# Kernel tuning notes

Measured on AMD Instinct MI355X. Metric: run time of the kernel, lower is better.

Reference implementation:

```python
import jax, jax.numpy as jnp
import numpy as np

N_COARSE = 64
N_FINE = 64
EPS = 1e-5

BS, N_RAYS = 1, 131072


def setup_inputs() -> dict:
    key = jax.random.key(0)
    k0, k1, k2, k3, k4, k5 = jax.random.split(key, 6)
    origins = jax.random.normal(k0, (BS, N_RAYS, 3), dtype=jnp.float32)
    dirs = jax.random.normal(k1, (BS, N_RAYS, 3), dtype=jnp.float32)
    dirs = dirs / jnp.linalg.norm(dirs, axis=-1, keepdims=True)
    near = 2.0 + 0.5 * jax.random.uniform(k2, (BS, N_RAYS, 1), dtype=jnp.float32)
    far = 6.0 + 0.5 * jax.random.uniform(k3, (BS, N_RAYS, 1), dtype=jnp.float32)
    rays = jnp.concatenate([origins, dirs, near, far], axis=-1)  # (bs, n_rays, 8)
    sigmas_coarse = jax.random.normal(k4, (BS, N_RAYS, N_COARSE), dtype=jnp.float32)
    rgbs_coarse = jax.random.uniform(k5, (BS, N_RAYS, N_COARSE, 3), dtype=jnp.float32)
    k6, k7 = jax.random.split(jax.random.fold_in(key, 1), 2)
    sigmas_fine = jax.random.normal(k6, (BS, N_RAYS, N_COARSE + N_FINE), dtype=jnp.float32)
    rgbs_fine = jax.random.uniform(k7, (BS, N_RAYS, N_COARSE + N_FINE, 3), dtype=jnp.float32)
    return {
        "rays": rays,
        "sigmas_coarse": sigmas_coarse,
        "rgbs_coarse": rgbs_coarse,
        "sigmas_fine": sigmas_fine,
        "rgbs_fine": rgbs_fine,
    }


def composite(rays, z_samp, sigmas, rgbs):
    """Alpha compositing along the sample axis (white background, far=inf)."""
    deltas = z_samp[..., 1:] - z_samp[..., :-1]
    delta_inf = jnp.full_like(deltas[..., :1], 1e10)
    deltas = jnp.concatenate([deltas, delta_inf], axis=-1)  # (bs, n_rays, K)
    alphas = 1.0 - jnp.exp(-deltas * jax.nn.relu(sigmas))
    shifted = jnp.concatenate(
        [jnp.ones_like(alphas[..., :1]), 1.0 - alphas + 1e-10], axis=-1)
    T = jnp.cumprod(shifted, axis=-1)  # transmittance
    weights = alphas * T[..., :-1]
    weights_sum = jnp.sum(weights, axis=-1, keepdims=True)
    rgb_final = jnp.sum(weights[..., None] * rgbs, axis=-2)
    depth_final = jnp.sum(weights * z_samp, axis=-1, keepdims=True)
    far = rays[..., 7:8]
    depth_final = depth_final + (1.0 - weights_sum) * far  # white_bkgd
    rgb_final = rgb_final + 1.0 - weights_sum
    return weights, rgb_final, depth_final, weights_sum


def sample_fine(bins, weights):
    """Deterministic inverse-CDF importance sampling (det=True, perturb=0)."""
    bs, n_rays = bins.shape[:2]
    w = jax.lax.stop_gradient(weights) + EPS  # (bs, n_rays, Kc-2)
    pdf = w / jnp.sum(w, axis=-1, keepdims=True)
    cdf = jnp.cumsum(pdf, axis=-1)
    cdf = jnp.concatenate([jnp.zeros_like(cdf[..., :1]), cdf], axis=-1)  # (.., Kc-1)
    u = jnp.broadcast_to(jnp.linspace(0.0, 1.0, N_FINE, dtype=cdf.dtype),
                         (bs, n_rays, N_FINE))
    n_bins = cdf.shape[-1]
    inds = jax.vmap(lambda c, uu: jnp.searchsorted(c, uu, side='right'))(
        cdf.reshape(-1, n_bins), u.reshape(-1, N_FINE)).reshape(bs, n_rays, N_FINE)
    below = jnp.maximum(inds - 1, 0)
    above = jnp.minimum(inds, N_COARSE - 2)
    cdf_b = jnp.take_along_axis(cdf, below, axis=-1)
    cdf_a = jnp.take_along_axis(cdf, above, axis=-1)
    bin_b = jnp.take_along_axis(bins, below, axis=-1)
    bin_a = jnp.take_along_axis(bins, above, axis=-1)
    denom = cdf_a - cdf_b
    denom = jnp.where(denom < EPS, 1.0, denom)
    z_fine = bin_b + (u - cdf_b) / denom * (bin_a - bin_b)
    return jax.lax.stop_gradient(z_fine)


def reference(rays, sigmas_coarse, rgbs_coarse, sigmas_fine, rgbs_fine):
    near, far = rays[..., 6:7], rays[..., 7:8]
    # sample_coarse, lindisp=True branch: linear blend of near/far, perturb=0
    step = 1.0 / N_COARSE
    t = jnp.linspace(0.0, 1.0 - step, N_COARSE, dtype=rays.dtype)
    z_coarse = near * (1.0 - t) + far * t  # (bs, n_rays, Kc)

    weights, rgbs, depths, alphas = composite(rays, z_coarse, sigmas_coarse, rgbs_coarse)

    bins = 0.5 * (z_coarse[..., :-1] + z_coarse[..., 1:])  # (.., Kc-1)
    z_fine = sample_fine(bins, weights[..., 1:-1])  # (.., Kf)
    z_combine = jnp.sort(jnp.concatenate([z_coarse, z_fine], axis=-1), axis=-1)

    weights_f, rgbs_f, depths_f, alphas_f = composite(rays, z_combine, sigmas_fine, rgbs_fine)
    # output dict: rgbs, alphas, depths (+ fine variants)
    return rgbs, alphas, depths, rgbs_f, alphas_f, depths_f
```

## Files before the change

### kernel.cpp

```cpp
#include <hip/hip_runtime.h>

#define EPS_F 1e-5f

#define DPPF(old, x, ctrl, rm, bm) \
  __int_as_float(__builtin_amdgcn_update_dpp(__float_as_int(old), __float_as_int(x), ctrl, rm, bm, false))

#define WAVE_SR1(old, x) DPPF(old, x, 0x138, 0xf, 0xf)

__device__ __forceinline__ float scan_add64(float x) {
  x += DPPF(0.0f, x, 0x111, 0xf, 0xf);
  x += DPPF(0.0f, x, 0x112, 0xf, 0xf);
  x += DPPF(0.0f, x, 0x114, 0xf, 0xf);
  x += DPPF(0.0f, x, 0x118, 0xf, 0xf);
  x += DPPF(0.0f, x, 0x142, 0xa, 0xf);
  x += DPPF(0.0f, x, 0x143, 0xc, 0xf);
  return x;
}
__device__ __forceinline__ float scan_mul64(float x) {
  x *= DPPF(1.0f, x, 0x111, 0xf, 0xf);
  x *= DPPF(1.0f, x, 0x112, 0xf, 0xf);
  x *= DPPF(1.0f, x, 0x114, 0xf, 0xf);
  x *= DPPF(1.0f, x, 0x118, 0xf, 0xf);
  x *= DPPF(1.0f, x, 0x142, 0xa, 0xf);
  x *= DPPF(1.0f, x, 0x143, 0xc, 0xf);
  return x;
}
__device__ __forceinline__ float wave_total(float x) {
  float s = scan_add64(x);
  return __int_as_float(__builtin_amdgcn_readlane(__float_as_int(s), 63));
}

__global__ __launch_bounds__(256) void nerf_volrend(
    const float* __restrict__ rays,
    const float* __restrict__ sigc,
    const float* __restrict__ rgbc,
    const float* __restrict__ sigf,
    const float* __restrict__ rgbf,
    float* __restrict__ out, int n_rays)
{
  const int wave = threadIdx.x >> 6;
  const int lane = threadIdx.x & 63;
  const int ray  = (blockIdx.x << 2) + wave;

  __shared__ float s_cdf[4][64];
  __shared__ int   s_cc [4][64];
  __shared__ float s_zcb[4][128];

  const float nearv = rays[ray*8 + 6];
  const float farv  = rays[ray*8 + 7];

  float sgv = sigc[ray*64 + lane];
  const float r0 = rgbc[ray*192 + lane*3 + 0];
  const float r1 = rgbc[ray*192 + lane*3 + 1];
  const float r2 = rgbc[ray*192 + lane*3 + 2];
  const float2 sgf = ((const float2*)(sigf + (size_t)ray*128))[lane];
  const float* rb = rgbf + (size_t)ray*384 + lane*6;
  const float2 rA = *(const float2*)(rb + 0);
  const float2 rB = *(const float2*)(rb + 2);
  const float2 rC = *(const float2*)(rb + 4);

  const float t  = (float)lane * 0.015625f;
  const float tn = (float)(lane + 1) * 0.015625f;
  const float z     = nearv * (1.0f - t)  + farv * t;
  const float znext = nearv * (1.0f - tn) + farv * tn;
  const float delta = (lane == 63) ? 1e10f : (znext - z);
  sgv = fmaxf(sgv, 0.0f);
  const float a  = 1.0f - __expf(-delta * sgv);
  const float sh = 1.0f - a + 1e-10f;

  const float pin = scan_mul64(sh);
  const float T   = WAVE_SR1(1.0f, pin);
  const float w   = a * T;

  const float rw = scan_add64(w * r0);
  const float gw = scan_add64(w * r1);
  const float bw = scan_add64(w * r2);
  const float dw = scan_add64(w * z);
  const float ws = scan_add64(w);

  if (lane == 63) {
    out[ray*3 + 0]      = rw + 1.0f - ws;
    out[ray*3 + 1]      = gw + 1.0f - ws;
    out[ray*3 + 2]      = bw + 1.0f - ws;
    out[n_rays*3 + ray] = ws;
    out[n_rays*4 + ray] = dw + (1.0f - ws) * farv;
  }

  const float wnext = __shfl_down(w, 1);
  const float wp    = (lane < 62) ? (wnext + EPS_F) : 0.0f;
  const float wpsum = wave_total(wp);
  const float csum  = scan_add64(wp / wpsum);

  if (lane < 62) s_cdf[wave][lane + 1] = csum;
  if (lane == 0) s_cdf[wave][0] = 0.0f;

  const float* cdf = s_cdf[wave];
  const float u = (lane == 63) ? 1.0f : (float)lane * (1.0f / 63.0f);
  int pos = 0;
  #pragma unroll
  for (int stp = 32; stp; stp >>= 1) {
    int np = pos + stp;
    if (np <= 63 && cdf[np - 1] <= u) pos = np;
  }
  const int below = max(pos - 1, 0);
  const int above = min(pos, 62);
  const float cdf_b = cdf[below], cdf_a = cdf[above];
  const float tb  = (float)below * 0.015625f, tb1 = (float)(below + 1) * 0.015625f;
  const float ta  = (float)above * 0.015625f, ta1 = (float)(above + 1) * 0.015625f;
  const float bin_b = 0.5f * ((nearv*(1.0f-tb)  + farv*tb)  + (nearv*(1.0f-tb1) + farv*tb1));
  const float bin_a = 0.5f * ((nearv*(1.0f-ta)  + farv*ta)  + (nearv*(1.0f-ta1) + farv*ta1));
  float dn = cdf_a - cdf_b;
  if (dn < EPS_F) dn = 1.0f;
  const float zf = bin_b + (u - cdf_b) / dn * (bin_a - bin_b);

  const float inv_step = 64.0f / (farv - nearv);
  int cc = (int)floorf((zf - nearv) * inv_step) + 1;
  cc = min(max(cc, 0), 64);
  s_cc[wave][lane] = cc;
  s_zcb[wave][lane + cc] = zf;

  const int* ccl = s_cc[wave];
  int cf = 0;
  #pragma unroll
  for (int stp = 64; stp; stp >>= 1) {
    int np = cf + stp;
    if (np <= 64 && ccl[np - 1] <= lane) cf = np;
  }
  s_zcb[wave][lane + cf] = z;

  const float* zcb = s_zcb[wave];
  const float2 zp = ((const float2*)zcb)[lane];
  const float z0 = zp.x, z1 = zp.y;
  const float z2 = zcb[(lane == 63) ? 127 : (2*lane + 2)];
  const float d0 = z1 - z0;
  const float d1 = (lane == 63) ? 1e10f : (z2 - z1);

  const float s0 = fmaxf(sgf.x, 0.0f);
  const float s1 = fmaxf(sgf.y, 0.0f);
  const float a0 = 1.0f - __expf(-d0 * s0);
  const float a1 = 1.0f - __expf(-d1 * s1);
  const float t0 = 1.0f - a0 + 1e-10f;
  const float t1 = 1.0f - a1 + 1e-10f;

  const float pp  = scan_mul64(t0 * t1);
  const float Pex = WAVE_SR1(1.0f, pp);
  const float w0 = a0 * Pex;
  const float w1 = a1 * Pex * t0;

  const float fR = scan_add64(w0 * rA.x + w1 * rB.y);
  const float fG = scan_add64(w0 * rA.y + w1 * rC.x);
  const float fB = scan_add64(w0 * rB.x + w1 * rC.y);
  const float fD = scan_add64(w0 * z0   + w1 * z1);
  const float fW = scan_add64(w0 + w1);

  if (lane == 63) {
    out[n_rays*5 + ray*3 + 0] = fR + 1.0f - fW;
    out[n_rays*5 + ray*3 + 1] = fG + 1.0f - fW;
    out[n_rays*5 + ray*3 + 2] = fB + 1.0f - fW;
    out[n_rays*8 + ray]       = fW;
    out[n_rays*9 + ray]       = fD + (1.0f - fW) * farv;
  }
}

extern "C" void kernel_launch(void* const* d_in, const int* in_sizes, int n_in,
                              void* d_out, int out_size, void* d_ws, size_t ws_size,
                              hipStream_t stream) {
  const float* rays = (const float*)d_in[0];
  const float* sigc = (const float*)d_in[1];
  const float* rgbc = (const float*)d_in[2];
  const float* sigf = (const float*)d_in[3];
  const float* rgbf = (const float*)d_in[4];
  float* out = (float*)d_out;
  const int n_rays = in_sizes[0] / 8;
  const int blocks = n_rays / 4;
  nerf_volrend<<<blocks, 256, 0, stream>>>(rays, sigc, rgbc, sigf, rgbf, out, n_rays);
}
```

Before: 406.5 us.

## Process two rays per wave with interleaved scans and derive weight sums algebraically

Each wave now handles two rays (A and B), interleaving their DPP scan chains so independent work can hide the latency of dependent cross-lane operations, and the grid is halved. The weight-sum scans are replaced by 1 minus the final transmittance product, which removes two scans per ray. This raises register pressure and LDS use per block, which may lower occupancy. The algebraic shortcut can differ slightly from the explicit sum because of the 1e-10 term added to each factor.

```diff
diff --git a/kernel.cpp b/kernel.cpp
--- a/kernel.cpp
+++ b/kernel.cpp
@@ -40,125 +40,198 @@
 {
   const int wave = threadIdx.x >> 6;
   const int lane = threadIdx.x & 63;
-  const int ray  = (blockIdx.x << 2) + wave;
-
-  __shared__ float s_cdf[4][64];
-  __shared__ int   s_cc [4][64];
-  __shared__ float s_zcb[4][128];
-
-  const float nearv = rays[ray*8 + 6];
-  const float farv  = rays[ray*8 + 7];
-
-  float sgv = sigc[ray*64 + lane];
-  const float r0 = rgbc[ray*192 + lane*3 + 0];
-  const float r1 = rgbc[ray*192 + lane*3 + 1];
-  const float r2 = rgbc[ray*192 + lane*3 + 2];
-  const float2 sgf = ((const float2*)(sigf + (size_t)ray*128))[lane];
-  const float* rb = rgbf + (size_t)ray*384 + lane*6;
-  const float2 rA = *(const float2*)(rb + 0);
-  const float2 rB = *(const float2*)(rb + 2);
-  const float2 rC = *(const float2*)(rb + 4);
+  const int rayA = (blockIdx.x << 3) + wave;
+  const int rayB = rayA + 4;
+
+  __shared__ float s_cdf[8][64];
+  __shared__ int   s_cc [8][64];
+  __shared__ float s_zcb[8][128];
+  const int ia = wave, ib = wave + 4;
+
+  const float nearA = rays[rayA*8 + 6], farA = rays[rayA*8 + 7];
+  const float nearB = rays[rayB*8 + 6], farB = rays[rayB*8 + 7];
+
+  float sgvA = sigc[rayA*64 + lane];
+  float sgvB = sigc[rayB*64 + lane];
+  const float r0A = rgbc[rayA*192 + lane*3 + 0];
+  const float r1A = rgbc[rayA*192 + lane*3 + 1];
+  const float r2A = rgbc[rayA*192 + lane*3 + 2];
+  const float r0B = rgbc[rayB*192 + lane*3 + 0];
+  const float r1B = rgbc[rayB*192 + lane*3 + 1];
+  const float r2B = rgbc[rayB*192 + lane*3 + 2];
+  const float2 sgfA = ((const float2*)(sigf + (size_t)rayA*128))[lane];
+  const float2 sgfB = ((const float2*)(sigf + (size_t)rayB*128))[lane];
+  const float* rbA = rgbf + (size_t)rayA*384 + lane*6;
+  const float* rbB = rgbf + (size_t)rayB*384 + lane*6;
+  const float2 cA0 = *(const float2*)(rbA + 0);
+  const float2 cA1 = *(const float2*)(rbA + 2);
+  const float2 cA2 = *(const float2*)(rbA + 4);
+  const float2 cB0 = *(const float2*)(rbB + 0);
+  const float2 cB1 = *(const float2*)(rbB + 2);
+  const float2 cB2 = *(const float2*)(rbB + 4);
 
   const float t  = (float)lane * 0.015625f;
   const float tn = (float)(lane + 1) * 0.015625f;
-  const float z     = nearv * (1.0f - t)  + farv * t;
-  const float znext = nearv * (1.0f - tn) + farv * tn;
-  const float delta = (lane == 63) ? 1e10f : (znext - z);
-  sgv = fmaxf(sgv, 0.0f);
-  const float a  = 1.0f - __expf(-delta * sgv);
-  const float sh = 1.0f - a + 1e-10f;
-
-  const float pin = scan_mul64(sh);
-  const float T   = WAVE_SR1(1.0f, pin);
-  const float w   = a * T;
-
-  const float rw = scan_add64(w * r0);
-  const float gw = scan_add64(w * r1);
-  const float bw = scan_add64(w * r2);
-  const float dw = scan_add64(w * z);
-  const float ws = scan_add64(w);
+  const float zA     = nearA * (1.0f - t)  + farA * t;
+  const float zB     = nearB * (1.0f - t)  + farB * t;
+  const float znxA   = nearA * (1.0f - tn) + farA * tn;
+  const float znxB   = nearB * (1.0f - tn) + farB * tn;
+  const float dltA = (lane == 63) ? 1e10f : (znxA - zA);
+  const float dltB = (lane == 63) ? 1e10f : (znxB - zB);
+  sgvA = fmaxf(sgvA, 0.0f);
+  sgvB = fmaxf(sgvB, 0.0f);
+  const float aA  = 1.0f - __expf(-dltA * sgvA);
+  const float aB  = 1.0f - __expf(-dltB * sgvB);
+  const float shA = 1.0f - aA + 1e-10f;
+  const float shB = 1.0f - aB + 1e-10f;
+
+  const float pinA = scan_mul64(shA);
+  const float pinB = scan_mul64(shB);
+  const float TA   = WAVE_SR1(1.0f, pinA);
+  const float TB   = WAVE_SR1(1.0f, pinB);
+  const float wA   = aA * TA;
+  const float wB   = aB * TB;
+
+  const float rwA = scan_add64(wA * r0A);
+  const float rwB = scan_add64(wB * r0B);
+  const float gwA = scan_add64(wA * r1A);
+  const float gwB = scan_add64(wB * r1B);
+  const float bwA = scan_add64(wA * r2A);
+  const float bwB = scan_add64(wB * r2B);
+  const float dwA = scan_add64(wA * zA);
+  const float dwB = scan_add64(wB * zB);
 
   if (lane == 63) {
-    out[ray*3 + 0]      = rw + 1.0f - ws;
-    out[ray*3 + 1]      = gw + 1.0f - ws;
-    out[ray*3 + 2]      = bw + 1.0f - ws;
-    out[n_rays*3 + ray] = ws;
-    out[n_rays*4 + ray] = dw + (1.0f - ws) * farv;
-  }
-
-  const float wnext = __shfl_down(w, 1);
-  const float wp    = (lane < 62) ? (wnext + EPS_F) : 0.0f;
-  const float wpsum = wave_total(wp);
-  const float csum  = scan_add64(wp / wpsum);
-
-  if (lane < 62) s_cdf[wave][lane + 1] = csum;
-  if (lane == 0) s_cdf[wave][0] = 0.0f;
-
-  const float* cdf = s_cdf[wave];
+    const float wsA = 1.0f - pinA;
+    const float wsB = 1.0f - pinB;
+    out[rayA*3 + 0]      = rwA + 1.0f - wsA;
+    out[rayA*3 + 1]      = gwA + 1.0f - wsA;
+    out[rayA*3 + 2]      = bwA + 1.0f - wsA;
+    out[n_rays*3 + rayA] = wsA;
+    out[n_rays*4 + rayA] = dwA + (1.0f - wsA) * farA;
+    out[rayB*3 + 0]      = rwB + 1.0f - wsB;
+    out[rayB*3 + 1]      = gwB + 1.0f - wsB;
+    out[rayB*3 + 2]      = bwB + 1.0f - wsB;
+    out[n_rays*3 + rayB] = wsB;
+    out[n_rays*4 + rayB] = dwB + (1.0f - wsB) * farB;
+  }
+
+  const float wnxA = __shfl_down(wA, 1);
+  const float wnxB = __shfl_down(wB, 1);
+  const float wpA  = (lane < 62) ? (wnxA + EPS_F) : 0.0f;
+  const float wpB  = (lane < 62) ? (wnxB + EPS_F) : 0.0f;
+  const float wpsA = wave_total(wpA);
+  const float wpsB = wave_total(wpB);
+  const float csA  = scan_add64(wpA / wpsA);
+  const float csB  = scan_add64(wpB / wpsB);
+
+  if (lane < 62) { s_cdf[ia][lane + 1] = csA; s_cdf[ib][lane + 1] = csB; }
+  if (lane == 0) { s_cdf[ia][0] = 0.0f;       s_cdf[ib][0] = 0.0f; }
+
+  const float* cdfA = s_cdf[ia];
+  const float* cdfB = s_cdf[ib];
   const float u = (lane == 63) ? 1.0f : (float)lane * (1.0f / 63.0f);
-  int pos = 0;
+  int posA = 0, posB = 0;
   #pragma unroll
   for (int stp = 32; stp; stp >>= 1) {
-    int np = pos + stp;
-    if (np <= 63 && cdf[np - 1] <= u) pos = np;
-  }
-  const int below = max(pos - 1, 0);
-  const int above = min(pos, 62);
-  const float cdf_b = cdf[below], cdf_a = cdf[above];
-  const float tb  = (float)below * 0.015625f, tb1 = (float)(below + 1) * 0.015625f;
-  const float ta  = (float)above * 0.015625f, ta1 = (float)(above + 1) * 0.015625f;
-  const float bin_b = 0.5f * ((nearv*(1.0f-tb)  + farv*tb)  + (nearv*(1.0f-tb1) + farv*tb1));
-  const float bin_a = 0.5f * ((nearv*(1.0f-ta)  + farv*ta)  + (nearv*(1.0f-ta1) + farv*ta1));
-  float dn = cdf_a - cdf_b;
-  if (dn < EPS_F) dn = 1.0f;
-  const float zf = bin_b + (u - cdf_b) / dn * (bin_a - bin_b);
-
-  const float inv_step = 64.0f / (farv - nearv);
-  int cc = (int)floorf((zf - nearv) * inv_step) + 1;
-  cc = min(max(cc, 0), 64);
-  s_cc[wave][lane] = cc;
-  s_zcb[wave][lane + cc] = zf;
-
-  const int* ccl = s_cc[wave];
-  int cf = 0;
+    int npA = posA + stp, npB = posB + stp;
+    if (npA <= 63 && cdfA[npA - 1] <= u) posA = npA;
+    if (npB <= 63 && cdfB[npB - 1] <= u) posB = npB;
+  }
+  const int belA = max(posA - 1, 0), abvA = min(posA, 62);
+  const int belB = max(posB - 1, 0), abvB = min(posB, 62);
+  const float cbA = cdfA[belA], caA = cdfA[abvA];
+  const float cbB = cdfB[belB], caB = cdfB[abvB];
+
+  const float tbA  = (float)belA * 0.015625f, tb1A = (float)(belA + 1) * 0.015625f;
+  const float taA  = (float)abvA * 0.015625f, ta1A = (float)(abvA + 1) * 0.015625f;
+  const float tbB  = (float)belB * 0.015625f, tb1B = (float)(belB + 1) * 0.015625f;
+  const float taB  = (float)abvB * 0.015625f, ta1B = (float)(abvB + 1) * 0.015625f;
+  const float binbA = 0.5f * ((nearA*(1.0f-tbA) + farA*tbA) + (nearA*(1.0f-tb1A) + farA*tb1A));
+  const float binaA = 0.5f * ((nearA*(1.0f-taA) + farA*taA) + (nearA*(1.0f-ta1A) + farA*ta1A));
+  const float binbB = 0.5f * ((nearB*(1.0f-tbB) + farB*tbB) + (nearB*(1.0f-tb1B) + farB*tb1B));
+  const float binaB = 0.5f * ((nearB*(1.0f-taB) + farB*taB) + (nearB*(1.0f-ta1B) + farB*ta1B));
+  float dnA = caA - cbA; if (dnA < EPS_F) dnA = 1.0f;
+  float dnB = caB - cbB; if (dnB < EPS_F) dnB = 1.0f;
+  const float zfA = binbA + (u - cbA) / dnA * (binaA - binbA);
+  const float zfB = binbB + (u - cbB) / dnB * (binaB - binbB);
+
+  const float invsA = 64.0f / (farA - nearA);
+  const float invsB = 64.0f / (farB - nearB);
+  int ccA = (int)floorf((zfA - nearA) * invsA) + 1;
+  int ccB = (int)floorf((zfB - nearB) * invsB) + 1;
+  ccA = min(max(ccA, 0), 64);
+  ccB = min(max(ccB, 0), 64);
+  s_cc[ia][lane] = ccA;
+  s_cc[ib][lane] = ccB;
+  s_zcb[ia][lane + ccA] = zfA;
+  s_zcb[ib][lane + ccB] = zfB;
+
+  const int* cclA = s_cc[ia];
+  const int* cclB = s_cc[ib];
+  int cfA = 0, cfB = 0;
   #pragma unroll
   for (int stp = 64; stp; stp >>= 1) {
-    int np = cf + stp;
-    if (np <= 64 && ccl[np - 1] <= lane) cf = np;
-  }
-  s_zcb[wave][lane + cf] = z;
-
-  const float* zcb = s_zcb[wave];
-  const float2 zp = ((const float2*)zcb)[lane];
-  const float z0 = zp.x, z1 = zp.y;
-  const float z2 = zcb[(lane == 63) ? 127 : (2*lane + 2)];
-  const float d0 = z1 - z0;
-  const float d1 = (lane == 63) ? 1e10f : (z2 - z1);
-
-  const float s0 = fmaxf(sgf.x, 0.0f);
-  const float s1 = fmaxf(sgf.y, 0.0f);
-  const float a0 = 1.0f - __expf(-d0 * s0);
-  const float a1 = 1.0f - __expf(-d1 * s1);
-  const float t0 = 1.0f - a0 + 1e-10f;
-  const float t1 = 1.0f - a1 + 1e-10f;
-
-  const float pp  = scan_mul64(t0 * t1);
-  const float Pex = WAVE_SR1(1.0f, pp);
-  const float w0 = a0 * Pex;
-  const float w1 = a1 * Pex * t0;
-
-  const float fR = scan_add64(w0 * rA.x + w1 * rB.y);
-  const float fG = scan_add64(w0 * rA.y + w1 * rC.x);
-  const float fB = scan_add64(w0 * rB.x + w1 * rC.y);
-  const float fD = scan_add64(w0 * z0   + w1 * z1);
-  const float fW = scan_add64(w0 + w1);
+    int npA = cfA + stp, npB = cfB + stp;
+    if (npA <= 64 && cclA[npA - 1] <= lane) cfA = npA;
+    if (npB <= 64 && cclB[npB - 1] <= lane) cfB = npB;
+  }
+  s_zcb[ia][lane + cfA] = zA;
+  s_zcb[ib][lane + cfB] = zB;
+
+  const float* zcbA = s_zcb[ia];
+  const float* zcbB = s_zcb[ib];
+  const float2 zpA = ((const float2*)zcbA)[lane];
+  const float2 zpB = ((const float2*)zcbB)[lane];
+  const float z0A = zpA.x, z1A = zpA.y;
+  const float z0B = zpB.x, z1B = zpB.y;
+  const float z2A = zcbA[(lane == 63) ? 127 : (2*lane + 2)];
+  const float z2B = zcbB[(lane == 63) ? 127 : (2*lane + 2)];
+  const float d0A = z1A - z0A;
+  const float d0B = z1B - z0B;
+  const float d1A = (lane == 63) ? 1e10f : (z2A - z1A);
+  const float d1B = (lane == 63) ? 1e10f : (z2B - z1B);
+
+  const float s0A = fmaxf(sgfA.x, 0.0f), s1A = fmaxf(sgfA.y, 0.0f);
+  const float s0B = fmaxf(sgfB.x, 0.0f), s1B = fmaxf(sgfB.y, 0.0f);
+  const float a0A = 1.0f - __expf(-d0A * s0A);
+  const float a1A = 1.0f - __expf(-d1A * s1A);
+  const float a0B = 1.0f - __expf(-d0B * s0B);
+  const float a1B = 1.0f - __expf(-d1B * s1B);
+  const float t0A = 1.0f - a0A + 1e-10f, t1A = 1.0f - a1A + 1e-10f;
+  const float t0B = 1.0f - a0B + 1e-10f, t1B = 1.0f - a1B + 1e-10f;
+
+  const float ppA  = scan_mul64(t0A * t1A);
+  const float ppB  = scan_mul64(t0B * t1B);
+  const float PexA = WAVE_SR1(1.0f, ppA);
+  const float PexB = WAVE_SR1(1.0f, ppB);
+  const float w0A = a0A * PexA;
+  const float w1A = a1A * PexA * t0A;
+  const float w0B = a0B * PexB;
+  const float w1B = a1B * PexB * t0B;
+
+  const float fRA = scan_add64(w0A * cA0.x + w1A * cA1.y);
+  const float fRB = scan_add64(w0B * cB0.x + w1B * cB1.y);
+  const float fGA = scan_add64(w0A * cA0.y + w1A * cA2.x);
+  const float fGB = scan_add64(w0B * cB0.y + w1B * cB2.x);
+  const float fBA = scan_add64(w0A * cA1.x + w1A * cA2.y);
+  const float fBB = scan_add64(w0B * cB1.x + w1B * cB2.y);
+  const float fDA = scan_add64(w0A * z0A  + w1A * z1A);
+  const float fDB = scan_add64(w0B * z0B  + w1B * z1B);
 
   if (lane == 63) {
-    out[n_rays*5 + ray*3 + 0] = fR + 1.0f - fW;
-    out[n_rays*5 + ray*3 + 1] = fG + 1.0f - fW;
-    out[n_rays*5 + ray*3 + 2] = fB + 1.0f - fW;
-    out[n_rays*8 + ray]       = fW;
-    out[n_rays*9 + ray]       = fD + (1.0f - fW) * farv;
+    const float fWA = 1.0f - ppA;
+    const float fWB = 1.0f - ppB;
+    out[n_rays*5 + rayA*3 + 0] = fRA + 1.0f - fWA;
+    out[n_rays*5 + rayA*3 + 1] = fGA + 1.0f - fWA;
+    out[n_rays*5 + rayA*3 + 2] = fBA + 1.0f - fWA;
+    out[n_rays*8 + rayA]       = fWA;
+    out[n_rays*9 + rayA]       = fDA + (1.0f - fWA) * farA;
+    out[n_rays*5 + rayB*3 + 0] = fRB + 1.0f - fWB;
+    out[n_rays*5 + rayB*3 + 1] = fGB + 1.0f - fWB;
+    out[n_rays*5 + rayB*3 + 2] = fBB + 1.0f - fWB;
+    out[n_rays*8 + rayB]       = fWB;
+    out[n_rays*9 + rayB]       = fDB + (1.0f - fWB) * farB;
   }
 }
 
@@ -172,6 +245,6 @@
   const float* rgbf = (const float*)d_in[4];
   float* out = (float*)d_out;
   const int n_rays = in_sizes[0] / 8;
-  const int blocks = n_rays / 4;
+  const int blocks = n_rays / 8;
   nerf_volrend<<<blocks, 256, 0, stream>>>(rays, sigc, rgbc, sigf, rgbf, out, n_rays);
 }
```

After: 407.9 us. About the same (+0.4%).
